# Optimization experiments

Hardware: AMD Instinct MI355X
Metric: run time of the kernel (lower is better)

## Reference

```python
import jax, jax.numpy as jnp
import numpy as np

N = 100000   # nodes
E = 1600000  # edges
EL = 200000  # decode pairs
D_IN, D_HID, D_OUT = 128, 128, 64


def setup_inputs() -> dict:
    key = jax.random.key(0)
    ks = jax.random.split(key, 9)
    x = jax.random.normal(ks[0], (N, D_IN), dtype=jnp.float32)
    edge_index = jax.random.randint(ks[1], (2, E), 0, N, dtype=jnp.int64)
    edge_label_index = jax.random.randint(ks[2], (2, EL), 0, N, dtype=jnp.int64)
    # GCNConv params: weight [in, out] (no bias inside linear), bias added after aggregation
    W1 = jax.random.normal(ks[3], (D_IN, D_HID), dtype=jnp.float32) / np.sqrt(D_IN)
    b1 = jnp.zeros((D_HID,), dtype=jnp.float32)
    W2 = jax.random.normal(ks[4], (D_HID, D_HID), dtype=jnp.float32) / np.sqrt(D_HID)
    b2 = jnp.zeros((D_HID,), dtype=jnp.float32)
    W3 = jax.random.normal(ks[5], (D_HID, D_OUT), dtype=jnp.float32) / np.sqrt(D_HID)
    b3 = jnp.zeros((D_OUT,), dtype=jnp.float32)
    return {"x": x, "edge_index": edge_index, "edge_label_index": edge_label_index,
            "W1": W1, "b1": b1, "W2": W2, "b2": b2, "W3": W3, "b3": b3}


def _gcn_norm(edge_index, num_nodes, dtype):
    # add self-loops, compute symmetric normalization deg^-1/2[src]*deg^-1/2[dst]
    loop = jnp.arange(num_nodes, dtype=edge_index.dtype)
    src = jnp.concatenate([edge_index[0], loop])
    dst = jnp.concatenate([edge_index[1], loop])
    deg = jax.ops.segment_sum(jnp.ones(src.shape, dtype=dtype), dst, num_segments=num_nodes)
    dinv = jax.lax.rsqrt(deg)  # deg >= 1 due to self-loops
    norm = dinv[src] * dinv[dst]
    return src, dst, norm


def _gcn_conv(h, W, b, src, dst, norm, num_nodes):
    h = h @ W                               # [N, out]
    msg = h[src] * norm[:, None]            # gather + scale  [E+N, out]
    out = jax.ops.segment_sum(msg, dst, num_segments=num_nodes)  # scatter-add
    return out + b


def reference(x, edge_index, edge_label_index, W1, b1, W2, b2, W3, b3):
    num_nodes = x.shape[0]
    src, dst, norm = _gcn_norm(edge_index, num_nodes, x.dtype)
    h = jax.nn.relu(_gcn_conv(x, W1, b1, src, dst, norm, num_nodes))
    h = jax.nn.relu(_gcn_conv(h, W2, b2, src, dst, norm, num_nodes))  # dropout is identity in eval
    z = _gcn_conv(h, W3, b3, src, dst, norm, num_nodes)
    # decode: dot product over candidate pairs
    return jnp.sum(z[edge_label_index[0]] * z[edge_label_index[1]], axis=-1)
```

## Files before the change

kernel.cpp:

```cpp
#include <hip/hip_runtime.h>
#include <hip/hip_bf16.h>

#define N_NODES 100000
#define N_EDGES 1600000
#define N_EL    200000

#define CPAD 16
#define GT_GEMM ((N_NODES + 63) / 64)
#define GR_RANK 782
#define GRID_FAT (3 * GR_RANK)
#define NB2 ((N_NODES + 511) / 512)
#define GF_FILL ((N_EDGES + 255) / 256)
#define GF_PRE  ((N_NODES + 1 + 3) / 4)

typedef unsigned int uint32;
typedef unsigned short ushort16;
typedef __attribute__((ext_vector_type(8))) short short8;
typedef __attribute__((ext_vector_type(4))) float f32x4;

static __device__ __forceinline__ ushort16 f2bf(float f) {
    uint32 u = __float_as_uint(f);
    u += 0x7fffu + ((u >> 16) & 1u);
    return (ushort16)(u >> 16);
}
static __device__ __forceinline__ float bf_lo(uint32 p) { return __uint_as_float(p << 16); }
static __device__ __forceinline__ float bf_hi(uint32 p) { return __uint_as_float(p & 0xffff0000u); }
static __device__ __forceinline__ float bf2f(ushort16 h) { return __uint_as_float((uint32)h << 16); }

__global__ void k_scanF(const int* __restrict__ cpad, int* __restrict__ lrp,
                        float* __restrict__ dinv, int* __restrict__ bsum,
                        int* __restrict__ boff, int* __restrict__ cnt) {
    __shared__ int s[512];
    __shared__ int lastflag;
    int t = threadIdx.x;
    int i = blockIdx.x * 512 + t;
    int v = (i < N_NODES) ? cpad[(size_t)i * CPAD] : 0;
    if (i < N_NODES) dinv[i] = 1.0f / sqrtf((float)(v + 1));
    s[t] = v;
    __syncthreads();
    for (int off = 1; off < 512; off <<= 1) {
        int u = (t >= off) ? s[t - off] : 0;
        __syncthreads();
        s[t] += u;
        __syncthreads();
    }
    if (i <= N_NODES) lrp[i] = s[t] - v;
    if (t == 0) {
        __hip_atomic_store(&bsum[blockIdx.x], s[511], __ATOMIC_RELEASE,
                           __HIP_MEMORY_SCOPE_AGENT);
        int c = __hip_atomic_fetch_add(cnt, 1, __ATOMIC_ACQ_REL,
                                       __HIP_MEMORY_SCOPE_AGENT);
        lastflag = (c == NB2 - 1);
    }
    __syncthreads();
    if (!lastflag) return;
    int bv = (t < NB2) ? __hip_atomic_load(&bsum[t], __ATOMIC_ACQUIRE,
                                           __HIP_MEMORY_SCOPE_AGENT) : 0;
    s[t] = bv;
    __syncthreads();
    for (int off = 1; off < 512; off <<= 1) {
        int u = (t >= off) ? s[t - off] : 0;
        __syncthreads();
        s[t] += u;
        __syncthreads();
    }
    if (t < NB2) boff[t] = s[t] - bv;
}

__global__ void k_fill2p(const int* __restrict__ src, const int* __restrict__ dst,
                         const int* __restrict__ lrp, const int* __restrict__ boff,
                         const int* __restrict__ r, int* __restrict__ col,
                         const float* __restrict__ dinv, uint32* __restrict__ t32) {
    unsigned bid = blockIdx.x;
    int tid = threadIdx.x;
    if (bid < GF_FILL) {
        int e = bid * 256 + tid;
        if (e >= N_EDGES) return;
        int dd = dst[e];
        int pos = lrp[dd] + boff[dd >> 9] + r[e];
        __builtin_nontemporal_store(src[e], &col[pos]);
    } else {
        int node = (bid - GF_FILL) * 4 + (tid >> 6);
        int lane = tid & 63;
        if (node > N_NODES) return;
        float di = (node < N_NODES) ? dinv[node] : 0.f;
        size_t idx = (size_t)node * 64 + lane;
        uint32 p = t32[idx];
        float lo = bf_lo(p) * di, hi = bf_hi(p) * di;
        t32[idx] = (uint32)f2bf(lo) | ((uint32)f2bf(hi) << 16);
    }
}

static __device__ __forceinline__ short8 load_afrag(const float* arow, int off) {
    float4 a0 = *(const float4*)(arow + off);
    float4 a1 = *(const float4*)(arow + off + 4);
    short8 af;
    af[0] = (short)f2bf(a0.x); af[1] = (short)f2bf(a0.y);
    af[2] = (short)f2bf(a0.z); af[3] = (short)f2bf(a0.w);
    af[4] = (short)f2bf(a1.x); af[5] = (short)f2bf(a1.y);
    af[6] = (short)f2bf(a1.z); af[7] = (short)f2bf(a1.w);
    return af;
}
static __device__ __forceinline__ short8 load_afrag(const ushort16* arow, int off) {
    return *(const short8*)(arow + off);
}

template <int D, typename AT, bool SCALE, int OS>
static __device__ __forceinline__ void gemm_body(int bid, const AT* __restrict__ A,
        const float* __restrict__ W, const float* __restrict__ dinv,
        ushort16* __restrict__ C) {
    constexpr int NT = D / 16;
    constexpr int LNT = (NT == 8) ? 3 : 2;
    __shared__ short sB[4 * NT * 64 * 8];

    int tid = threadIdx.x;

    constexpr int COMBOS = 4 * 4 * NT * 16;
    for (int cc = tid; cc < COMBOS; cc += 256) {
        int nn = cc & 15;
        int nt = (cc >> 4) & (NT - 1);
        int q  = (cc >> (4 + LNT)) & 3;
        int kt = cc >> (6 + LNT);
        short8 pk;
#pragma unroll
        for (int j = 0; j < 8; ++j)
            pk[j] = (short)f2bf(W[(kt * 32 + q * 8 + j) * D + nt * 16 + nn]);
        *(short8*)&sB[(((kt * NT + nt) * 64) + q * 16 + nn) * 8] = pk;
    }
    __syncthreads();

    int w = tid >> 6;
    int l = tid & 63;
    int q = l >> 4;
    int nn15 = l & 15;
    int m0 = bid * 64 + w * 16;

    f32x4 acc[NT];
#pragma unroll
    for (int i = 0; i < NT; ++i) acc[i] = (f32x4){0.f, 0.f, 0.f, 0.f};

    int m = m0 + nn15;
    m = min(m, N_NODES - 1);
    const AT* arow = A + (size_t)m * 128;

#pragma unroll
    for (int kt = 0; kt < 4; ++kt) {
        short8 af = load_afrag(arow, kt * 32 + q * 8);
#pragma unroll
        for (int nt = 0; nt < NT; ++nt) {
            short8 bf = *(const short8*)&sB[((kt * NT + nt) * 64 + l) * 8];
            acc[nt] = __builtin_amdgcn_mfma_f32_16x16x32_bf16(af, bf, acc[nt], 0, 0, 0);
        }
    }

    float4 dv;
    if constexpr (SCALE) dv = *(const float4*)(dinv + m0 + 4 * q);
    const float* dvp = (const float*)&dv;
#pragma unroll
    for (int nt = 0; nt < NT; ++nt) {
#pragma unroll
        for (int r = 0; r < 4; ++r) {
            int node = m0 + q * 4 + r;
            if (node < N_NODES) {
                float val = acc[nt][r];
                if constexpr (SCALE) val *= dvp[r];
                C[(size_t)node * OS + nt * 16 + nn15] = f2bf(val);
            }
        }
    }
}

template <int D, typename AT, bool SCALE, int OS>
__global__ __launch_bounds__(256, 5) void k_gemm_mfma(const AT* __restrict__ A,
        const float* __restrict__ W, const float* __restrict__ dinv,
        ushort16* __restrict__ C) {
    gemm_body<D, AT, SCALE, OS>(blockIdx.x, A, W, dinv, C);
}

__global__ __launch_bounds__(256, 5) void k_fat1(const float* __restrict__ A,
        const float* __restrict__ W, ushort16* __restrict__ C,
        const int* __restrict__ dst, int* __restrict__ cpad, int* __restrict__ r) {
    unsigned bid = blockIdx.x;
    unsigned g = bid / 3u;
    unsigned rem = bid - g * 3u;
    if (rem < 2u) {
        unsigned gid = g * 2u + rem;
        if (gid < GT_GEMM)
            gemm_body<128, float, false, 128>(gid, A, W, nullptr, C);
    } else {
        unsigned e0 = g * 2048u + threadIdx.x;
        int d[8], rr[8];
#pragma unroll
        for (int k = 0; k < 8; ++k) {
            unsigned e = e0 + k * 256u;
            if (e < N_EDGES) d[k] = dst[e];
        }
#pragma unroll
        for (int k = 0; k < 8; ++k) {
            unsigned e = e0 + k * 256u;
            if (e < N_EDGES) rr[k] = atomicAdd(&cpad[(size_t)d[k] * CPAD], 1);
        }
#pragma unroll
        for (int k = 0; k < 8; ++k) {
            unsigned e = e0 + k * 256u;
            if (e < N_EDGES) __builtin_nontemporal_store(rr[k], &r[e]);
        }
    }
}

template <bool RELU>
__global__ void k_gather128(const int* __restrict__ lrp, const int* __restrict__ boff,
                            const int* __restrict__ col, const float* __restrict__ dinv,
                            const uint32* __restrict__ t, const float* __restrict__ b,
                            uint32* __restrict__ outbuf) {
    __shared__ int sc[4][64];
    int tid = threadIdx.x;
    unsigned wid = (blockIdx.x * 256u + tid) >> 6;
    if (wid >= N_NODES) return;
    int w = tid >> 6;
    int lane = tid & 63;
    int beg = lrp[wid] + boff[wid >> 9];
    int end = lrp[wid + 1] + boff[(wid + 1) >> 9];
    float di = dinv[wid];
    uint32 p = t[(size_t)wid * 64 + lane];
    float ax = bf_lo(p), ay = bf_hi(p);
    for (int base = beg; base < end; base += 64) {
        int cnt = min(end - base, 64);
        int c = N_NODES;
        if (lane < cnt) c = col[base + lane];
        sc[w][lane] = c;
        int nb = (cnt + 7) >> 3;
        for (int j8 = 0; j8 < nb; ++j8) {
            int j = j8 << 3;
            int s0 = sc[w][j+0], s1 = sc[w][j+1], s2 = sc[w][j+2], s3 = sc[w][j+3];
            int s4 = sc[w][j+4], s5 = sc[w][j+5], s6 = sc[w][j+6], s7 = sc[w][j+7];
            uint32 v0 = t[(size_t)s0 * 64 + lane];
            uint32 v1 = t[(size_t)s1 * 64 + lane];
            uint32 v2 = t[(size_t)s2 * 64 + lane];
            uint32 v3 = t[(size_t)s3 * 64 + lane];
            uint32 v4 = t[(size_t)s4 * 64 + lane];
            uint32 v5 = t[(size_t)s5 * 64 + lane];
            uint32 v6 = t[(size_t)s6 * 64 + lane];
            uint32 v7 = t[(size_t)s7 * 64 + lane];
            ax += (bf_lo(v0) + bf_lo(v1)) + (bf_lo(v2) + bf_lo(v3))
                + ((bf_lo(v4) + bf_lo(v5)) + (bf_lo(v6) + bf_lo(v7)));
            ay += (bf_hi(v0) + bf_hi(v1)) + (bf_hi(v2) + bf_hi(v3))
                + ((bf_hi(v4) + bf_hi(v5)) + (bf_hi(v6) + bf_hi(v7)));
        }
    }
    float2 bb = ((const float2*)b)[lane];
    float ox = di * ax + bb.x;
    float oy = di * ay + bb.y;
    if (RELU) { ox = fmaxf(ox, 0.f); oy = fmaxf(oy, 0.f); }
    __builtin_nontemporal_store((uint32)f2bf(ox) | ((uint32)f2bf(oy) << 16),
                                &outbuf[(size_t)wid * 64 + lane]);
}

template <bool RELU>
__global__ void k_gather64(const int* __restrict__ lrp, const int* __restrict__ boff,
                           const int* __restrict__ col, const float* __restrict__ dinv,
                           const ushort16* __restrict__ t, const float* __restrict__ b,
                           ushort16* __restrict__ outbuf) {
    __shared__ int sc[4][64];
    int tid = threadIdx.x;
    unsigned wid = (blockIdx.x * 256u + tid) >> 6;
    if (wid >= N_NODES) return;
    int w = tid >> 6;
    int lane = tid & 63;
    int beg = lrp[wid] + boff[wid >> 9];
    int end = lrp[wid + 1] + boff[(wid + 1) >> 9];
    float di = dinv[wid];
    float acc = bf2f(t[(size_t)wid * 128 + lane]);
    for (int base = beg; base < end; base += 64) {
        int cnt = min(end - base, 64);
        int c = N_NODES;
        if (lane < cnt) c = col[base + lane];
        sc[w][lane] = c;
        int nb = (cnt + 7) >> 3;
        for (int j8 = 0; j8 < nb; ++j8) {
            int j = j8 << 3;
            int s0 = sc[w][j+0], s1 = sc[w][j+1], s2 = sc[w][j+2], s3 = sc[w][j+3];
            int s4 = sc[w][j+4], s5 = sc[w][j+5], s6 = sc[w][j+6], s7 = sc[w][j+7];
            float v0 = bf2f(t[(size_t)s0 * 128 + lane]);
            float v1 = bf2f(t[(size_t)s1 * 128 + lane]);
            float v2 = bf2f(t[(size_t)s2 * 128 + lane]);
            float v3 = bf2f(t[(size_t)s3 * 128 + lane]);
            float v4 = bf2f(t[(size_t)s4 * 128 + lane]);
            float v5 = bf2f(t[(size_t)s5 * 128 + lane]);
            float v6 = bf2f(t[(size_t)s6 * 128 + lane]);
            float v7 = bf2f(t[(size_t)s7 * 128 + lane]);
            acc += (v0 + v1) + (v2 + v3) + ((v4 + v5) + (v6 + v7));
        }
    }
    float o = di * acc + b[lane];
    if (RELU) o = fmaxf(o, 0.f);
    __builtin_nontemporal_store(f2bf(o), &outbuf[(size_t)wid * 64 + lane]);
}

__global__ void k_decode(const int* __restrict__ eli, const ushort16* __restrict__ z,
                         float* __restrict__ out) {
    int e = blockIdx.x * blockDim.x + threadIdx.x;
    if (e >= N_EL) return;
    int a = eli[e];
    int b = eli[N_EL + e];
    const uint4* za = (const uint4*)(z + (size_t)a * 64);
    const uint4* zb = (const uint4*)(z + (size_t)b * 64);
    float acc = 0.0f;
#pragma unroll
    for (int i = 0; i < 8; ++i) {
        uint4 va = za[i], vb = zb[i];
        acc += bf_lo(va.x) * bf_lo(vb.x) + bf_hi(va.x) * bf_hi(vb.x);
        acc += bf_lo(va.y) * bf_lo(vb.y) + bf_hi(va.y) * bf_hi(vb.y);
        acc += bf_lo(va.z) * bf_lo(vb.z) + bf_hi(va.z) * bf_hi(vb.z);
        acc += bf_lo(va.w) * bf_lo(vb.w) + bf_hi(va.w) * bf_hi(vb.w);
    }
    out[e] = acc;
}

extern "C" void kernel_launch(void* const* d_in, const int* in_sizes, int n_in,
                              void* d_out, int out_size, void* d_ws, size_t ws_size,
                              hipStream_t stream) {
    const float* x   = (const float*)d_in[0];
    const int*   ei  = (const int*)d_in[1];
    const int*   eli = (const int*)d_in[2];
    const float* W1  = (const float*)d_in[3];
    const float* b1  = (const float*)d_in[4];
    const float* W2  = (const float*)d_in[5];
    const float* b2  = (const float*)d_in[6];
    const float* W3  = (const float*)d_in[7];
    const float* b3  = (const float*)d_in[8];
    float* out = (float*)d_out;

    const int* srcA = ei;
    const int* dstA = ei + N_EDGES;

    char* ws = (char*)d_ws;
    float*    dinv   = (float*)   (ws + 0);
    int*      lrp    = (int*)     (ws + (1024u << 10));
    int*      bsum   = (int*)     (ws + (1888u << 10));
    int*      boff   = (int*)     (ws + (1896u << 10));
    int*      col    = (int*)     (ws + (2048u << 10));
    int*      r      = (int*)     (ws + (9u << 20));
    ushort16* t      = (ushort16*)(ws + (16u << 20));
    ushort16* aggb   = (ushort16*)(ws + (48u << 20));
    int*      cpad   = (int*)     (ws + (80u << 20));
    int*      cnt    = cpad + (size_t)N_NODES * CPAD;

    const int B = 256;
    const int gG  = (N_NODES * 64 + B - 1) / B;
    const int gEL = (N_EL + B - 1) / B;

    hipMemsetAsync(cpad, 0, ((size_t)N_NODES * CPAD + 16) * sizeof(int), stream);
    k_fat1<<<GRID_FAT, B, 0, stream>>>(x, W1, t, dstA, cpad, r);
    k_scanF<<<NB2, 512, 0, stream>>>(cpad, lrp, dinv, bsum, boff, cnt);
    k_fill2p<<<GF_FILL + GF_PRE, B, 0, stream>>>(srcA, dstA, lrp, boff, r, col,
                                                 dinv, (uint32*)t);

    k_gather128<true><<<gG, B, 0, stream>>>(lrp, boff, col, dinv, (const uint32*)t,
                                            b1, (uint32*)aggb);
    k_gemm_mfma<128, ushort16, true, 128><<<GT_GEMM, B, 0, stream>>>(aggb, W2, dinv, t);
    k_gather128<true><<<gG, B, 0, stream>>>(lrp, boff, col, dinv, (const uint32*)t,
                                            b2, (uint32*)aggb);
    k_gemm_mfma<64, ushort16, true, 128><<<GT_GEMM, B, 0, stream>>>(aggb, W3, dinv, t);
    k_gather64<false><<<gG, B, 0, stream>>>(lrp, boff, col, dinv, t, b3, aggb);

    k_decode<<<gEL, B, 0, stream>>>(eli, aggb, out);
}
```

Baseline: 437.2 us.

## Build CSR via two-level bucket sort and widen gather loads

```diff
diff --git a/kernel.cpp b/kernel.cpp
--- a/kernel.cpp
+++ b/kernel.cpp
@@ -5,13 +5,12 @@
 #define N_EDGES 1600000
 #define N_EL    200000
 
-#define CPAD 16
+#define NBKT 782
+#define NCHK 782
+#define CHKE 2048
+#define DCAP 2688
 #define GT_GEMM ((N_NODES + 63) / 64)
-#define GR_RANK 782
-#define GRID_FAT (3 * GR_RANK)
-#define NB2 ((N_NODES + 511) / 512)
-#define GF_FILL ((N_EDGES + 255) / 256)
-#define GF_PRE  ((N_NODES + 1 + 3) / 4)
+#define GRID_FAT (3 * NCHK)
 
 typedef unsigned int uint32;
 typedef unsigned short ushort16;
@@ -25,69 +24,147 @@
 }
 static __device__ __forceinline__ float bf_lo(uint32 p) { return __uint_as_float(p << 16); }
 static __device__ __forceinline__ float bf_hi(uint32 p) { return __uint_as_float(p & 0xffff0000u); }
-static __device__ __forceinline__ float bf2f(ushort16 h) { return __uint_as_float((uint32)h << 16); }
-
-__global__ void k_scanF(const int* __restrict__ cpad, int* __restrict__ lrp,
-                        float* __restrict__ dinv, int* __restrict__ bsum,
-                        int* __restrict__ boff, int* __restrict__ cnt) {
-    __shared__ int s[512];
+static __device__ __forceinline__ uint32 pack2(float lo, float hi) {
+    return (uint32)f2bf(lo) | ((uint32)f2bf(hi) << 16);
+}
+
+template <bool AT>
+static __device__ __forceinline__ int scan782(const int* __restrict__ in,
+                                              int* __restrict__ outv,
+                                              int* s, int tid) {
+    __syncthreads();
+    int v[4]; int sum = 0;
+    int i0 = tid * 4;
+#pragma unroll
+    for (int i = 0; i < 4; ++i) {
+        int idx = i0 + i;
+        int x = 0;
+        if (idx < NBKT)
+            x = AT ? __hip_atomic_load(&in[idx], __ATOMIC_ACQUIRE,
+                                       __HIP_MEMORY_SCOPE_AGENT)
+                   : in[idx];
+        v[i] = x; sum += x;
+    }
+    s[tid] = sum;
+    __syncthreads();
+    for (int off = 1; off < 256; off <<= 1) {
+        int u = (tid >= off) ? s[tid - off] : 0;
+        __syncthreads();
+        s[tid] += u;
+        __syncthreads();
+    }
+    int excl = s[tid] - sum;
+    int total = s[255];
+    int run = excl;
+#pragma unroll
+    for (int i = 0; i < 4; ++i) {
+        int idx = i0 + i;
+        if (idx < NBKT) outv[idx] = run;
+        run += v[i];
+    }
+    return total;
+}
+
+__global__ __launch_bounds__(256) void k_scanB(const int* __restrict__ H,
+        int* __restrict__ CO, int* __restrict__ TT, int* __restrict__ BB,
+        int* __restrict__ cnt) {
+    __shared__ int s[256];
     __shared__ int lastflag;
-    int t = threadIdx.x;
-    int i = blockIdx.x * 512 + t;
-    int v = (i < N_NODES) ? cpad[(size_t)i * CPAD] : 0;
-    if (i < N_NODES) dinv[i] = 1.0f / sqrtf((float)(v + 1));
-    s[t] = v;
-    __syncthreads();
-    for (int off = 1; off < 512; off <<= 1) {
-        int u = (t >= off) ? s[t - off] : 0;
-        __syncthreads();
-        s[t] += u;
-        __syncthreads();
-    }
-    if (i <= N_NODES) lrp[i] = s[t] - v;
-    if (t == 0) {
-        __hip_atomic_store(&bsum[blockIdx.x], s[511], __ATOMIC_RELEASE,
-                           __HIP_MEMORY_SCOPE_AGENT);
+    int b = blockIdx.x, tid = threadIdx.x;
+    int total = scan782<false>(H + (size_t)b * NBKT, CO + (size_t)b * NBKT, s, tid);
+    if (tid == 0) {
+        __hip_atomic_store(&TT[b], total, __ATOMIC_RELEASE, __HIP_MEMORY_SCOPE_AGENT);
         int c = __hip_atomic_fetch_add(cnt, 1, __ATOMIC_ACQ_REL,
                                        __HIP_MEMORY_SCOPE_AGENT);
-        lastflag = (c == NB2 - 1);
+        lastflag = (c == NBKT - 1);
     }
     __syncthreads();
     if (!lastflag) return;
-    int bv = (t < NB2) ? __hip_atomic_load(&bsum[t], __ATOMIC_ACQUIRE,
-                                           __HIP_MEMORY_SCOPE_AGENT) : 0;
-    s[t] = bv;
-    __syncthreads();
-    for (int off = 1; off < 512; off <<= 1) {
-        int u = (t >= off) ? s[t - off] : 0;
-        __syncthreads();
-        s[t] += u;
-        __syncthreads();
-    }
-    if (t < NB2) boff[t] = s[t] - bv;
-}
-
-__global__ void k_fill2p(const int* __restrict__ src, const int* __restrict__ dst,
-                         const int* __restrict__ lrp, const int* __restrict__ boff,
-                         const int* __restrict__ r, int* __restrict__ col,
-                         const float* __restrict__ dinv, uint32* __restrict__ t32) {
-    unsigned bid = blockIdx.x;
-    int tid = threadIdx.x;
-    if (bid < GF_FILL) {
-        int e = bid * 256 + tid;
-        if (e >= N_EDGES) return;
-        int dd = dst[e];
-        int pos = lrp[dd] + boff[dd >> 9] + r[e];
-        __builtin_nontemporal_store(src[e], &col[pos]);
-    } else {
-        int node = (bid - GF_FILL) * 4 + (tid >> 6);
-        int lane = tid & 63;
-        if (node > N_NODES) return;
-        float di = (node < N_NODES) ? dinv[node] : 0.f;
-        size_t idx = (size_t)node * 64 + lane;
-        uint32 p = t32[idx];
-        float lo = bf_lo(p) * di, hi = bf_hi(p) * di;
-        t32[idx] = (uint32)f2bf(lo) | ((uint32)f2bf(hi) << 16);
+    int gt = scan782<true>(TT, BB, s, tid);
+    __syncthreads();
+    if (tid == 0) BB[NBKT] = gt;
+}
+
+__global__ __launch_bounds__(256) void k_csrC(const int* __restrict__ src,
+        const int* __restrict__ dst, const int* __restrict__ CO,
+        const int* __restrict__ BB, long long* __restrict__ ed) {
+    __shared__ int cur[NBKT];
+    int c = blockIdx.x, tid = threadIdx.x;
+    for (int i = tid; i < NBKT; i += 256)
+        cur[i] = BB[i] + CO[(size_t)i * NBKT + c];
+    __syncthreads();
+    int e0 = c * CHKE;
+#pragma unroll
+    for (int kk = 0; kk < 8; ++kk) {
+        int e = e0 + kk * 256 + tid;
+        if (e < N_EDGES) {
+            int sE = src[e], dE = dst[e];
+            int pos = atomicAdd(&cur[dE >> 7], 1);
+            long long pv = (unsigned int)sE | ((long long)(unsigned int)dE << 32);
+            __builtin_nontemporal_store(pv, &ed[pos]);
+        }
+    }
+}
+
+__global__ __launch_bounds__(256) void k_csrD(const long long* __restrict__ ed,
+        const int* __restrict__ BB, int* __restrict__ rowptr,
+        float* __restrict__ dinv, int* __restrict__ col, uint32* __restrict__ t32) {
+    __shared__ long long eds[DCAP];
+    __shared__ int deg[128], scn[128], cur[128];
+    __shared__ float dv[128];
+    int b = blockIdx.x, tid = threadIdx.x;
+    int base = BB[b], lim = BB[b + 1];
+    int n = lim - base;
+    bool cached = (n <= DCAP);
+    if (tid < 128) deg[tid] = 0;
+    __syncthreads();
+    for (int i = tid; i < n; i += 256) {
+        long long e = ed[base + i];
+        if (cached) eds[i] = e;
+        int d = (int)(e >> 32);
+        atomicAdd(&deg[d & 127], 1);
+    }
+    __syncthreads();
+    if (tid < 128) scn[tid] = deg[tid];
+    __syncthreads();
+    for (int off = 1; off < 128; off <<= 1) {
+        int u = 0;
+        if (tid < 128 && tid >= off) u = scn[tid - off];
+        __syncthreads();
+        if (tid < 128) scn[tid] += u;
+        __syncthreads();
+    }
+    if (tid < 128) {
+        int excl = scn[tid] - deg[tid];
+        cur[tid] = excl;
+        int node = b * 128 + tid;
+        if (node < N_NODES) {
+            rowptr[node] = base + excl;
+            float di = rsqrtf((float)(deg[tid] + 1));
+            dinv[node] = di;
+            dv[tid] = di;
+        }
+    }
+    if (b == NBKT - 1 && tid == 0) rowptr[N_NODES] = BB[NBKT];
+    __syncthreads();
+    for (int i = tid; i < n; i += 256) {
+        long long e = cached ? eds[i] : ed[base + i];
+        int sE = (int)(e & 0xffffffff);
+        int d = (int)(e >> 32);
+        int p = atomicAdd(&cur[d & 127], 1);
+        col[base + p] = sE;
+    }
+    __syncthreads();
+    for (int idx = tid; idx < 128 * 64; idx += 256) {
+        int ni = idx >> 6;
+        int node = b * 128 + ni;
+        if (node < N_NODES) {
+            int k = idx & 63;
+            size_t a = (size_t)node * 64 + k;
+            uint32 p = t32[a];
+            float di = dv[ni];
+            t32[a] = pack2(bf_lo(p) * di, bf_hi(p) * di);
+        }
     }
 }
 
@@ -108,11 +185,9 @@
 template <int D, typename AT, bool SCALE, int OS>
 static __device__ __forceinline__ void gemm_body(int bid, const AT* __restrict__ A,
         const float* __restrict__ W, const float* __restrict__ dinv,
-        ushort16* __restrict__ C) {
+        ushort16* __restrict__ C, short* sB) {
     constexpr int NT = D / 16;
     constexpr int LNT = (NT == 8) ? 3 : 2;
-    __shared__ short sB[4 * NT * 64 * 8];
-
     int tid = threadIdx.x;
 
     constexpr int COMBOS = 4 * 4 * NT * 16;
@@ -153,9 +228,9 @@
         }
     }
 
-    float4 dv;
-    if constexpr (SCALE) dv = *(const float4*)(dinv + m0 + 4 * q);
-    const float* dvp = (const float*)&dv;
+    float4 dvv;
+    if constexpr (SCALE) dvv = *(const float4*)(dinv + m0 + 4 * q);
+    const float* dvp = (const float*)&dvv;
 #pragma unroll
     for (int nt = 0; nt < NT; ++nt) {
 #pragma unroll
@@ -174,56 +249,56 @@
 __global__ __launch_bounds__(256, 5) void k_gemm_mfma(const AT* __restrict__ A,
         const float* __restrict__ W, const float* __restrict__ dinv,
         ushort16* __restrict__ C) {
-    gemm_body<D, AT, SCALE, OS>(blockIdx.x, A, W, dinv, C);
+    __shared__ short sB[4 * (D / 16) * 64 * 8];
+    gemm_body<D, AT, SCALE, OS>(blockIdx.x, A, W, dinv, C, sB);
 }
 
 __global__ __launch_bounds__(256, 5) void k_fat1(const float* __restrict__ A,
         const float* __restrict__ W, ushort16* __restrict__ C,
-        const int* __restrict__ dst, int* __restrict__ cpad, int* __restrict__ r) {
+        const int* __restrict__ dst, int* __restrict__ H) {
+    __shared__ __align__(16) char smem[32768];
     unsigned bid = blockIdx.x;
     unsigned g = bid / 3u;
     unsigned rem = bid - g * 3u;
+    int tid = threadIdx.x;
     if (rem < 2u) {
         unsigned gid = g * 2u + rem;
         if (gid < GT_GEMM)
-            gemm_body<128, float, false, 128>(gid, A, W, nullptr, C);
+            gemm_body<128, float, false, 128>(gid, A, W, nullptr, C, (short*)smem);
     } else {
-        unsigned e0 = g * 2048u + threadIdx.x;
-        int d[8], rr[8];
-#pragma unroll
-        for (int k = 0; k < 8; ++k) {
-            unsigned e = e0 + k * 256u;
-            if (e < N_EDGES) d[k] = dst[e];
-        }
-#pragma unroll
-        for (int k = 0; k < 8; ++k) {
-            unsigned e = e0 + k * 256u;
-            if (e < N_EDGES) rr[k] = atomicAdd(&cpad[(size_t)d[k] * CPAD], 1);
-        }
-#pragma unroll
-        for (int k = 0; k < 8; ++k) {
-            unsigned e = e0 + k * 256u;
-            if (e < N_EDGES) __builtin_nontemporal_store(rr[k], &r[e]);
-        }
+        int* hist = (int*)smem;
+        for (int i = tid; i < NBKT; i += 256) hist[i] = 0;
+        __syncthreads();
+        int e0 = (int)g * CHKE;
+#pragma unroll
+        for (int kk = 0; kk < 8; ++kk) {
+            int e = e0 + kk * 256 + tid;
+            if (e < N_EDGES) atomicAdd(&hist[dst[e] >> 7], 1);
+        }
+        __syncthreads();
+        for (int i = tid; i < NBKT; i += 256)
+            H[(size_t)i * NBKT + g] = hist[i];
     }
 }
 
 template <bool RELU>
-__global__ void k_gather128(const int* __restrict__ lrp, const int* __restrict__ boff,
-                            const int* __restrict__ col, const float* __restrict__ dinv,
-                            const uint32* __restrict__ t, const float* __restrict__ b,
-                            uint32* __restrict__ outbuf) {
+__global__ void k_gather128(const int* __restrict__ rowptr, const int* __restrict__ col,
+                            const float* __restrict__ dinv, const uint32* __restrict__ t,
+                            const float* __restrict__ b, uint32* __restrict__ outbuf) {
     __shared__ int sc[4][64];
     int tid = threadIdx.x;
     unsigned wid = (blockIdx.x * 256u + tid) >> 6;
     if (wid >= N_NODES) return;
     int w = tid >> 6;
     int lane = tid & 63;
-    int beg = lrp[wid] + boff[wid >> 9];
-    int end = lrp[wid + 1] + boff[(wid + 1) >> 9];
-    float di = dinv[wid];
-    uint32 p = t[(size_t)wid * 64 + lane];
-    float ax = bf_lo(p), ay = bf_hi(p);
+    int h = lane >> 5;
+    int k = lane & 31;
+    int beg = rowptr[wid], end = rowptr[wid + 1];
+    float a0 = 0.f, a1 = 0.f, a2 = 0.f, a3 = 0.f;
+    if (h == 0) {
+        uint2 p = ((const uint2*)(t + (size_t)wid * 64))[k];
+        a0 = bf_lo(p.x); a1 = bf_hi(p.x); a2 = bf_lo(p.y); a3 = bf_hi(p.y);
+    }
     for (int base = beg; base < end; base += 64) {
         int cnt = min(end - base, 64);
         int c = N_NODES;
@@ -232,45 +307,59 @@
         int nb = (cnt + 7) >> 3;
         for (int j8 = 0; j8 < nb; ++j8) {
             int j = j8 << 3;
-            int s0 = sc[w][j+0], s1 = sc[w][j+1], s2 = sc[w][j+2], s3 = sc[w][j+3];
-            int s4 = sc[w][j+4], s5 = sc[w][j+5], s6 = sc[w][j+6], s7 = sc[w][j+7];
-            uint32 v0 = t[(size_t)s0 * 64 + lane];
-            uint32 v1 = t[(size_t)s1 * 64 + lane];
-            uint32 v2 = t[(size_t)s2 * 64 + lane];
-            uint32 v3 = t[(size_t)s3 * 64 + lane];
-            uint32 v4 = t[(size_t)s4 * 64 + lane];
-            uint32 v5 = t[(size_t)s5 * 64 + lane];
-            uint32 v6 = t[(size_t)s6 * 64 + lane];
-            uint32 v7 = t[(size_t)s7 * 64 + lane];
-            ax += (bf_lo(v0) + bf_lo(v1)) + (bf_lo(v2) + bf_lo(v3))
-                + ((bf_lo(v4) + bf_lo(v5)) + (bf_lo(v6) + bf_lo(v7)));
-            ay += (bf_hi(v0) + bf_hi(v1)) + (bf_hi(v2) + bf_hi(v3))
-                + ((bf_hi(v4) + bf_hi(v5)) + (bf_hi(v6) + bf_hi(v7)));
-        }
-    }
-    float2 bb = ((const float2*)b)[lane];
-    float ox = di * ax + bb.x;
-    float oy = di * ay + bb.y;
-    if (RELU) { ox = fmaxf(ox, 0.f); oy = fmaxf(oy, 0.f); }
-    __builtin_nontemporal_store((uint32)f2bf(ox) | ((uint32)f2bf(oy) << 16),
-                                &outbuf[(size_t)wid * 64 + lane]);
-}
-
-template <bool RELU>
-__global__ void k_gather64(const int* __restrict__ lrp, const int* __restrict__ boff,
-                           const int* __restrict__ col, const float* __restrict__ dinv,
-                           const ushort16* __restrict__ t, const float* __restrict__ b,
-                           ushort16* __restrict__ outbuf) {
+            int r0 = sc[w][j + 0 + h];
+            int r1 = sc[w][j + 2 + h];
+            int r2 = sc[w][j + 4 + h];
+            int r3 = sc[w][j + 6 + h];
+            uint2 v0 = ((const uint2*)(t + (size_t)r0 * 64))[k];
+            uint2 v1 = ((const uint2*)(t + (size_t)r1 * 64))[k];
+            uint2 v2 = ((const uint2*)(t + (size_t)r2 * 64))[k];
+            uint2 v3 = ((const uint2*)(t + (size_t)r3 * 64))[k];
+            a0 += (bf_lo(v0.x) + bf_lo(v1.x)) + (bf_lo(v2.x) + bf_lo(v3.x));
+            a1 += (bf_hi(v0.x) + bf_hi(v1.x)) + (bf_hi(v2.x) + bf_hi(v3.x));
+            a2 += (bf_lo(v0.y) + bf_lo(v1.y)) + (bf_lo(v2.y) + bf_lo(v3.y));
+            a3 += (bf_hi(v0.y) + bf_hi(v1.y)) + (bf_hi(v2.y) + bf_hi(v3.y));
+        }
+    }
+    a0 += __shfl_xor(a0, 32);
+    a1 += __shfl_xor(a1, 32);
+    a2 += __shfl_xor(a2, 32);
+    a3 += __shfl_xor(a3, 32);
+    if (h == 0) {
+        float di = dinv[wid];
+        float4 bb = ((const float4*)b)[k];
+        float o0 = fmaf(di, a0, bb.x);
+        float o1 = fmaf(di, a1, bb.y);
+        float o2 = fmaf(di, a2, bb.z);
+        float o3 = fmaf(di, a3, bb.w);
+        if (RELU) {
+            o0 = fmaxf(o0, 0.f); o1 = fmaxf(o1, 0.f);
+            o2 = fmaxf(o2, 0.f); o3 = fmaxf(o3, 0.f);
+        }
+        unsigned long long pv = (unsigned long long)pack2(o0, o1)
+                              | ((unsigned long long)pack2(o2, o3) << 32);
+        __builtin_nontemporal_store(pv,
+            (unsigned long long*)(outbuf + (size_t)wid * 64) + k);
+    }
+}
+
+__global__ void k_gather64(const int* __restrict__ rowptr, const int* __restrict__ col,
+                           const float* __restrict__ dinv, const uint32* __restrict__ t,
+                           const float* __restrict__ b, uint32* __restrict__ outbuf) {
     __shared__ int sc[4][64];
     int tid = threadIdx.x;
     unsigned wid = (blockIdx.x * 256u + tid) >> 6;
     if (wid >= N_NODES) return;
     int w = tid >> 6;
     int lane = tid & 63;
-    int beg = lrp[wid] + boff[wid >> 9];
-    int end = lrp[wid + 1] + boff[(wid + 1) >> 9];
-    float di = dinv[wid];
-    float acc = bf2f(t[(size_t)wid * 128 + lane]);
+    int h = lane >> 4;
+    int k = lane & 15;
+    int beg = rowptr[wid], end = rowptr[wid + 1];
+    float a0 = 0.f, a1 = 0.f, a2 = 0.f, a3 = 0.f;
+    if (h == 0) {
+        uint2 p = ((const uint2*)(t + (size_t)wid * 64))[k];
+        a0 = bf_lo(p.x); a1 = bf_hi(p.x); a2 = bf_lo(p.y); a3 = bf_hi(p.y);
+    }
     for (int base = beg; base < end; base += 64) {
         int cnt = min(end - base, 64);
         int c = N_NODES;
@@ -279,22 +368,32 @@
         int nb = (cnt + 7) >> 3;
         for (int j8 = 0; j8 < nb; ++j8) {
             int j = j8 << 3;
-            int s0 = sc[w][j+0], s1 = sc[w][j+1], s2 = sc[w][j+2], s3 = sc[w][j+3];
-            int s4 = sc[w][j+4], s5 = sc[w][j+5], s6 = sc[w][j+6], s7 = sc[w][j+7];
-            float v0 = bf2f(t[(size_t)s0 * 128 + lane]);
-            float v1 = bf2f(t[(size_t)s1 * 128 + lane]);
-            float v2 = bf2f(t[(size_t)s2 * 128 + lane]);
-            float v3 = bf2f(t[(size_t)s3 * 128 + lane]);
-            float v4 = bf2f(t[(size_t)s4 * 128 + lane]);
-            float v5 = bf2f(t[(size_t)s5 * 128 + lane]);
-            float v6 = bf2f(t[(size_t)s6 * 128 + lane]);
-            float v7 = bf2f(t[(size_t)s7 * 128 + lane]);
-            acc += (v0 + v1) + (v2 + v3) + ((v4 + v5) + (v6 + v7));
-        }
-    }
-    float o = di * acc + b[lane];
-    if (RELU) o = fmaxf(o, 0.f);
-    __builtin_nontemporal_store(f2bf(o), &outbuf[(size_t)wid * 64 + lane]);
+            int r0 = sc[w][j + h];
+            int r1 = sc[w][j + 4 + h];
+            uint2 v0 = ((const uint2*)(t + (size_t)r0 * 64))[k];
+            uint2 v1 = ((const uint2*)(t + (size_t)r1 * 64))[k];
+            a0 += bf_lo(v0.x) + bf_lo(v1.x);
+            a1 += bf_hi(v0.x) + bf_hi(v1.x);
+            a2 += bf_lo(v0.y) + bf_lo(v1.y);
+            a3 += bf_hi(v0.y) + bf_hi(v1.y);
+        }
+    }
+    a0 += __shfl_xor(a0, 16); a0 += __shfl_xor(a0, 32);
+    a1 += __shfl_xor(a1, 16); a1 += __shfl_xor(a1, 32);
+    a2 += __shfl_xor(a2, 16); a2 += __shfl_xor(a2, 32);
+    a3 += __shfl_xor(a3, 16); a3 += __shfl_xor(a3, 32);
+    if (h == 0) {
+        float di = dinv[wid];
+        float4 bb = ((const float4*)b)[k];
+        float o0 = fmaf(di, a0, bb.x);
+        float o1 = fmaf(di, a1, bb.y);
+        float o2 = fmaf(di, a2, bb.z);
+        float o3 = fmaf(di, a3, bb.w);
+        unsigned long long pv = (unsigned long long)pack2(o0, o1)
+                              | ((unsigned long long)pack2(o2, o3) << 32);
+        __builtin_nontemporal_store(pv,
+            (unsigned long long*)(outbuf + (size_t)wid * 32) + k);
+    }
 }
 
 __global__ void k_decode(const int* __restrict__ eli, const ushort16* __restrict__ z,
@@ -335,34 +434,38 @@
     const int* dstA = ei + N_EDGES;
 
     char* ws = (char*)d_ws;
-    float*    dinv   = (float*)   (ws + 0);
-    int*      lrp    = (int*)     (ws + (1024u << 10));
-    int*      bsum   = (int*)     (ws + (1888u << 10));
-    int*      boff   = (int*)     (ws + (1896u << 10));
-    int*      col    = (int*)     (ws + (2048u << 10));
-    int*      r      = (int*)     (ws + (9u << 20));
-    ushort16* t      = (ushort16*)(ws + (16u << 20));
-    ushort16* aggb   = (ushort16*)(ws + (48u << 20));
-    int*      cpad   = (int*)     (ws + (80u << 20));
-    int*      cnt    = cpad + (size_t)N_NODES * CPAD;
+    float*      dinv   = (float*)    (ws + 0);
+    int*        rowptr = (int*)      (ws + (1024u << 10));
+    int*        TT     = (int*)      (ws + (1536u << 10));
+    int*        BB     = (int*)      (ws + (1638u << 10));
+    int*        cnt    = (int*)      (ws + (1792u << 10));
+    int*        col    = (int*)      (ws + (2048u << 10));
+    int*        H      = (int*)      (ws + (9u << 20));
+    int*        CO     = (int*)      (ws + (12u << 20));
+    long long*  ed     = (long long*)(ws + (16u << 20));
+    ushort16*   t      = (ushort16*) (ws + (32u << 20));
+    ushort16*   aggb   = (ushort16*) (ws + (60u << 20));
 
     const int B = 256;
     const int gG  = (N_NODES * 64 + B - 1) / B;
     const int gEL = (N_EL + B - 1) / B;
 
-    hipMemsetAsync(cpad, 0, ((size_t)N_NODES * CPAD + 16) * sizeof(int), stream);
-    k_fat1<<<GRID_FAT, B, 0, stream>>>(x, W1, t, dstA, cpad, r);
-    k_scanF<<<NB2, 512, 0, stream>>>(cpad, lrp, dinv, bsum, boff, cnt);
-    k_fill2p<<<GF_FILL + GF_PRE, B, 0, stream>>>(srcA, dstA, lrp, boff, r, col,
-                                                 dinv, (uint32*)t);
-
-    k_gather128<true><<<gG, B, 0, stream>>>(lrp, boff, col, dinv, (const uint32*)t,
+    hipMemsetAsync(cnt, 0, 4, stream);
+    hipMemsetAsync((char*)t + (size_t)N_NODES * 256, 0, 256, stream);
+
+    k_fat1<<<GRID_FAT, B, 0, stream>>>(x, W1, t, dstA, H);
+    k_scanB<<<NBKT, B, 0, stream>>>(H, CO, TT, BB, cnt);
+    k_csrC<<<NCHK, B, 0, stream>>>(srcA, dstA, CO, BB, ed);
+    k_csrD<<<NBKT, B, 0, stream>>>(ed, BB, rowptr, dinv, col, (uint32*)t);
+
+    k_gather128<true><<<gG, B, 0, stream>>>(rowptr, col, dinv, (const uint32*)t,
                                             b1, (uint32*)aggb);
     k_gemm_mfma<128, ushort16, true, 128><<<GT_GEMM, B, 0, stream>>>(aggb, W2, dinv, t);
-    k_gather128<true><<<gG, B, 0, stream>>>(lrp, boff, col, dinv, (const uint32*)t,
+    k_gather128<true><<<gG, B, 0, stream>>>(rowptr, col, dinv, (const uint32*)t,
                                             b2, (uint32*)aggb);
     k_gemm_mfma<64, ushort16, true, 128><<<GT_GEMM, B, 0, stream>>>(aggb, W3, dinv, t);
-    k_gather64<false><<<gG, B, 0, stream>>>(lrp, boff, col, dinv, t, b3, aggb);
+    k_gather64<<<gG, B, 0, stream>>>(rowptr, col, dinv, (const uint32*)t, b3,
+                                     (uint32*)aggb);
 
     k_decode<<<gEL, B, 0, stream>>>(eli, aggb, out);
 }
```

Measured after the change: 461.7 us. +5.6%, slower.

## Split gather rows across half-waves, fold dinv scaling into first gather, compact layer-3 output

Applied to the files above, without the earlier changes.

```diff
diff --git a/kernel.cpp b/kernel.cpp
--- a/kernel.cpp
+++ b/kernel.cpp
@@ -7,11 +7,8 @@
 
 #define CPAD 16
 #define GT_GEMM ((N_NODES + 63) / 64)
-#define GR_RANK 782
-#define GRID_FAT (3 * GR_RANK)
+#define GE_RANK ((N_EDGES + 255) / 256)
 #define NB2 ((N_NODES + 511) / 512)
-#define GF_FILL ((N_EDGES + 255) / 256)
-#define GF_PRE  ((N_NODES + 1 + 3) / 4)
 
 typedef unsigned int uint32;
 typedef unsigned short ushort16;
@@ -25,7 +22,9 @@
 }
 static __device__ __forceinline__ float bf_lo(uint32 p) { return __uint_as_float(p << 16); }
 static __device__ __forceinline__ float bf_hi(uint32 p) { return __uint_as_float(p & 0xffff0000u); }
-static __device__ __forceinline__ float bf2f(ushort16 h) { return __uint_as_float((uint32)h << 16); }
+static __device__ __forceinline__ uint32 pack2(float lo, float hi) {
+    return (uint32)f2bf(lo) | ((uint32)f2bf(hi) << 16);
+}
 
 __global__ void k_scanF(const int* __restrict__ cpad, int* __restrict__ lrp,
                         float* __restrict__ dinv, int* __restrict__ bsum,
@@ -35,7 +34,7 @@
     int t = threadIdx.x;
     int i = blockIdx.x * 512 + t;
     int v = (i < N_NODES) ? cpad[(size_t)i * CPAD] : 0;
-    if (i < N_NODES) dinv[i] = 1.0f / sqrtf((float)(v + 1));
+    if (i < N_NODES) dinv[i] = rsqrtf((float)(v + 1));
     s[t] = v;
     __syncthreads();
     for (int off = 1; off < 512; off <<= 1) {
@@ -67,28 +66,14 @@
     if (t < NB2) boff[t] = s[t] - bv;
 }
 
-__global__ void k_fill2p(const int* __restrict__ src, const int* __restrict__ dst,
-                         const int* __restrict__ lrp, const int* __restrict__ boff,
-                         const int* __restrict__ r, int* __restrict__ col,
-                         const float* __restrict__ dinv, uint32* __restrict__ t32) {
-    unsigned bid = blockIdx.x;
-    int tid = threadIdx.x;
-    if (bid < GF_FILL) {
-        int e = bid * 256 + tid;
-        if (e >= N_EDGES) return;
-        int dd = dst[e];
-        int pos = lrp[dd] + boff[dd >> 9] + r[e];
-        __builtin_nontemporal_store(src[e], &col[pos]);
-    } else {
-        int node = (bid - GF_FILL) * 4 + (tid >> 6);
-        int lane = tid & 63;
-        if (node > N_NODES) return;
-        float di = (node < N_NODES) ? dinv[node] : 0.f;
-        size_t idx = (size_t)node * 64 + lane;
-        uint32 p = t32[idx];
-        float lo = bf_lo(p) * di, hi = bf_hi(p) * di;
-        t32[idx] = (uint32)f2bf(lo) | ((uint32)f2bf(hi) << 16);
-    }
+__global__ void k_fill2(const int* __restrict__ src, const int* __restrict__ dst,
+                        const int* __restrict__ lrp, const int* __restrict__ boff,
+                        const int* __restrict__ r, int* __restrict__ col) {
+    int e = blockIdx.x * blockDim.x + threadIdx.x;
+    if (e >= N_EDGES) return;
+    int dd = dst[e];
+    int pos = lrp[dd] + boff[dd >> 9] + r[e];
+    __builtin_nontemporal_store(src[e], &col[pos]);
 }
 
 static __device__ __forceinline__ short8 load_afrag(const float* arow, int off) {
@@ -108,11 +93,9 @@
 template <int D, typename AT, bool SCALE, int OS>
 static __device__ __forceinline__ void gemm_body(int bid, const AT* __restrict__ A,
         const float* __restrict__ W, const float* __restrict__ dinv,
-        ushort16* __restrict__ C) {
+        ushort16* __restrict__ C, short* sB) {
     constexpr int NT = D / 16;
     constexpr int LNT = (NT == 8) ? 3 : 2;
-    __shared__ short sB[4 * NT * 64 * 8];
-
     int tid = threadIdx.x;
 
     constexpr int COMBOS = 4 * 4 * NT * 16;
@@ -153,148 +136,185 @@
         }
     }
 
-    float4 dv;
-    if constexpr (SCALE) dv = *(const float4*)(dinv + m0 + 4 * q);
-    const float* dvp = (const float*)&dv;
+    float4 dvv;
+    if constexpr (SCALE) dvv = *(const float4*)(dinv + m0 + 4 * q);
+    const float* dvp = (const float*)&dvv;
 #pragma unroll
     for (int nt = 0; nt < NT; ++nt) {
 #pragma unroll
-        for (int r = 0; r < 4; ++r) {
-            int node = m0 + q * 4 + r;
+        for (int rr = 0; rr < 4; ++rr) {
+            int node = m0 + q * 4 + rr;
             if (node < N_NODES) {
-                float val = acc[nt][r];
-                if constexpr (SCALE) val *= dvp[r];
+                float val = acc[nt][rr];
+                if constexpr (SCALE) val *= dvp[rr];
                 C[(size_t)node * OS + nt * 16 + nn15] = f2bf(val);
             }
         }
     }
 }
 
-template <int D, typename AT, bool SCALE, int OS>
+template <int D, typename AT, bool SCALE, int OS, bool PADZ>
 __global__ __launch_bounds__(256, 5) void k_gemm_mfma(const AT* __restrict__ A,
         const float* __restrict__ W, const float* __restrict__ dinv,
         ushort16* __restrict__ C) {
-    gemm_body<D, AT, SCALE, OS>(blockIdx.x, A, W, dinv, C);
+    __shared__ short sB[4 * (D / 16) * 64 * 8];
+    if (PADZ && blockIdx.x == 0 && threadIdx.x < OS / 2)
+        ((uint32*)C)[(size_t)N_NODES * (OS / 2) + threadIdx.x] = 0;
+    gemm_body<D, AT, SCALE, OS>(blockIdx.x, A, W, dinv, C, sB);
 }
 
 __global__ __launch_bounds__(256, 5) void k_fat1(const float* __restrict__ A,
         const float* __restrict__ W, ushort16* __restrict__ C,
         const int* __restrict__ dst, int* __restrict__ cpad, int* __restrict__ r) {
+    __shared__ short sB[4 * 8 * 64 * 8];
     unsigned bid = blockIdx.x;
-    unsigned g = bid / 3u;
-    unsigned rem = bid - g * 3u;
-    if (rem < 2u) {
-        unsigned gid = g * 2u + rem;
-        if (gid < GT_GEMM)
-            gemm_body<128, float, false, 128>(gid, A, W, nullptr, C);
+    unsigned g = bid / 5u;
+    unsigned rem = bid - g * 5u;
+    if (rem == 0u) {
+        gemm_body<128, float, false, 128>(g, A, W, nullptr, C, sB);
     } else {
-        unsigned e0 = g * 2048u + threadIdx.x;
-        int d[8], rr[8];
-#pragma unroll
-        for (int k = 0; k < 8; ++k) {
-            unsigned e = e0 + k * 256u;
-            if (e < N_EDGES) d[k] = dst[e];
-        }
-#pragma unroll
-        for (int k = 0; k < 8; ++k) {
-            unsigned e = e0 + k * 256u;
-            if (e < N_EDGES) rr[k] = atomicAdd(&cpad[(size_t)d[k] * CPAD], 1);
-        }
-#pragma unroll
-        for (int k = 0; k < 8; ++k) {
-            unsigned e = e0 + k * 256u;
-            if (e < N_EDGES) __builtin_nontemporal_store(rr[k], &r[e]);
-        }
-    }
-}
-
-template <bool RELU>
+        unsigned rid = g * 4u + rem - 1u;
+        unsigned e = rid * 256u + threadIdx.x;
+        if (e < N_EDGES) r[e] = atomicAdd(&cpad[(size_t)dst[e] * CPAD], 1);
+    }
+}
+
+template <bool RELU, bool WEIGHTED>
 __global__ void k_gather128(const int* __restrict__ lrp, const int* __restrict__ boff,
                             const int* __restrict__ col, const float* __restrict__ dinv,
                             const uint32* __restrict__ t, const float* __restrict__ b,
                             uint32* __restrict__ outbuf) {
+    __shared__ int   sc[4][64];
+    __shared__ float sd[4][64];
+    int tid = threadIdx.x;
+    unsigned wid = (blockIdx.x * 256u + tid) >> 6;
+    if (wid >= N_NODES) return;
+    int w = tid >> 6;
+    int lane = tid & 63;
+    int h = lane >> 5;
+    int k = lane & 31;
+    int beg = lrp[wid] + boff[wid >> 9];
+    int end = lrp[wid + 1] + boff[(wid + 1) >> 9];
+    float di = dinv[wid];
+    float a0 = 0.f, a1 = 0.f, a2 = 0.f, a3 = 0.f;
+    if (h == 0) {
+        uint2 p = ((const uint2*)(t + (size_t)wid * 64))[k];
+        float sw = WEIGHTED ? di : 1.0f;
+        a0 = sw * bf_lo(p.x); a1 = sw * bf_hi(p.x);
+        a2 = sw * bf_lo(p.y); a3 = sw * bf_hi(p.y);
+    }
+    for (int base = beg; base < end; base += 64) {
+        int cnt = min(end - base, 64);
+        int c = WEIGHTED ? 0 : N_NODES;
+        if (lane < cnt) c = col[base + lane];
+        sc[w][lane] = c;
+        if (WEIGHTED) sd[w][lane] = (lane < cnt) ? dinv[c] : 0.f;
+        int nb8 = (cnt + 7) >> 3;
+        for (int j8 = 0; j8 < nb8; ++j8) {
+            int j = j8 << 3;
+            int r0 = sc[w][j + 0 + h];
+            int r1 = sc[w][j + 2 + h];
+            int r2 = sc[w][j + 4 + h];
+            int r3 = sc[w][j + 6 + h];
+            uint2 v0 = ((const uint2*)(t + (size_t)r0 * 64))[k];
+            uint2 v1 = ((const uint2*)(t + (size_t)r1 * 64))[k];
+            uint2 v2 = ((const uint2*)(t + (size_t)r2 * 64))[k];
+            uint2 v3 = ((const uint2*)(t + (size_t)r3 * 64))[k];
+            if (WEIGHTED) {
+                float d0 = sd[w][j + 0 + h];
+                float d1 = sd[w][j + 2 + h];
+                float d2 = sd[w][j + 4 + h];
+                float d3 = sd[w][j + 6 + h];
+                a0 = fmaf(d0, bf_lo(v0.x), a0); a1 = fmaf(d0, bf_hi(v0.x), a1);
+                a2 = fmaf(d0, bf_lo(v0.y), a2); a3 = fmaf(d0, bf_hi(v0.y), a3);
+                a0 = fmaf(d1, bf_lo(v1.x), a0); a1 = fmaf(d1, bf_hi(v1.x), a1);
+                a2 = fmaf(d1, bf_lo(v1.y), a2); a3 = fmaf(d1, bf_hi(v1.y), a3);
+                a0 = fmaf(d2, bf_lo(v2.x), a0); a1 = fmaf(d2, bf_hi(v2.x), a1);
+                a2 = fmaf(d2, bf_lo(v2.y), a2); a3 = fmaf(d2, bf_hi(v2.y), a3);
+                a0 = fmaf(d3, bf_lo(v3.x), a0); a1 = fmaf(d3, bf_hi(v3.x), a1);
+                a2 = fmaf(d3, bf_lo(v3.y), a2); a3 = fmaf(d3, bf_hi(v3.y), a3);
+            } else {
+                a0 += (bf_lo(v0.x) + bf_lo(v1.x)) + (bf_lo(v2.x) + bf_lo(v3.x));
+                a1 += (bf_hi(v0.x) + bf_hi(v1.x)) + (bf_hi(v2.x) + bf_hi(v3.x));
+                a2 += (bf_lo(v0.y) + bf_lo(v1.y)) + (bf_lo(v2.y) + bf_lo(v3.y));
+                a3 += (bf_hi(v0.y) + bf_hi(v1.y)) + (bf_hi(v2.y) + bf_hi(v3.y));
+            }
+        }
+    }
+    a0 += __shfl_xor(a0, 32);
+    a1 += __shfl_xor(a1, 32);
+    a2 += __shfl_xor(a2, 32);
+    a3 += __shfl_xor(a3, 32);
+    if (h == 0) {
+        float4 bb = ((const float4*)b)[k];
+        float o0 = fmaf(di, a0, bb.x);
+        float o1 = fmaf(di, a1, bb.y);
+        float o2 = fmaf(di, a2, bb.z);
+        float o3 = fmaf(di, a3, bb.w);
+        if (RELU) {
+            o0 = fmaxf(o0, 0.f); o1 = fmaxf(o1, 0.f);
+            o2 = fmaxf(o2, 0.f); o3 = fmaxf(o3, 0.f);
+        }
+        unsigned long long pv = (unsigned long long)pack2(o0, o1)
+                              | ((unsigned long long)pack2(o2, o3) << 32);
+        __builtin_nontemporal_store(pv,
+            (unsigned long long*)(outbuf + (size_t)wid * 64) + k);
+    }
+}
+
+__global__ void k_gather64(const int* __restrict__ lrp, const int* __restrict__ boff,
+                           const int* __restrict__ col, const float* __restrict__ dinv,
+                           const uint32* __restrict__ z, const float* __restrict__ b,
+                           uint32* __restrict__ outbuf) {
     __shared__ int sc[4][64];
     int tid = threadIdx.x;
     unsigned wid = (blockIdx.x * 256u + tid) >> 6;
     if (wid >= N_NODES) return;
     int w = tid >> 6;
     int lane = tid & 63;
+    int h = lane >> 4;
+    int k = lane & 15;
     int beg = lrp[wid] + boff[wid >> 9];
     int end = lrp[wid + 1] + boff[(wid + 1) >> 9];
-    float di = dinv[wid];
-    uint32 p = t[(size_t)wid * 64 + lane];
-    float ax = bf_lo(p), ay = bf_hi(p);
+    float a0 = 0.f, a1 = 0.f, a2 = 0.f, a3 = 0.f;
+    if (h == 0) {
+        uint2 p = ((const uint2*)(z + (size_t)wid * 32))[k];
+        a0 = bf_lo(p.x); a1 = bf_hi(p.x); a2 = bf_lo(p.y); a3 = bf_hi(p.y);
+    }
     for (int base = beg; base < end; base += 64) {
         int cnt = min(end - base, 64);
         int c = N_NODES;
         if (lane < cnt) c = col[base + lane];
         sc[w][lane] = c;
-        int nb = (cnt + 7) >> 3;
-        for (int j8 = 0; j8 < nb; ++j8) {
+        int nb8 = (cnt + 7) >> 3;
+        for (int j8 = 0; j8 < nb8; ++j8) {
             int j = j8 << 3;
-            int s0 = sc[w][j+0], s1 = sc[w][j+1], s2 = sc[w][j+2], s3 = sc[w][j+3];
-            int s4 = sc[w][j+4], s5 = sc[w][j+5], s6 = sc[w][j+6], s7 = sc[w][j+7];
-            uint32 v0 = t[(size_t)s0 * 64 + lane];
-            uint32 v1 = t[(size_t)s1 * 64 + lane];
-            uint32 v2 = t[(size_t)s2 * 64 + lane];
-            uint32 v3 = t[(size_t)s3 * 64 + lane];
-            uint32 v4 = t[(size_t)s4 * 64 + lane];
-            uint32 v5 = t[(size_t)s5 * 64 + lane];
-            uint32 v6 = t[(size_t)s6 * 64 + lane];
-            uint32 v7 = t[(size_t)s7 * 64 + lane];
-            ax += (bf_lo(v0) + bf_lo(v1)) + (bf_lo(v2) + bf_lo(v3))
-                + ((bf_lo(v4) + bf_lo(v5)) + (bf_lo(v6) + bf_lo(v7)));
-            ay += (bf_hi(v0) + bf_hi(v1)) + (bf_hi(v2) + bf_hi(v3))
-                + ((bf_hi(v4) + bf_hi(v5)) + (bf_hi(v6) + bf_hi(v7)));
-        }
-    }
-    float2 bb = ((const float2*)b)[lane];
-    float ox = di * ax + bb.x;
-    float oy = di * ay + bb.y;
-    if (RELU) { ox = fmaxf(ox, 0.f); oy = fmaxf(oy, 0.f); }
-    __builtin_nontemporal_store((uint32)f2bf(ox) | ((uint32)f2bf(oy) << 16),
-                                &outbuf[(size_t)wid * 64 + lane]);
-}
-
-template <bool RELU>
-__global__ void k_gather64(const int* __restrict__ lrp, const int* __restrict__ boff,
-                           const int* __restrict__ col, const float* __restrict__ dinv,
-                           const ushort16* __restrict__ t, const float* __restrict__ b,
-                           ushort16* __restrict__ outbuf) {
-    __shared__ int sc[4][64];
-    int tid = threadIdx.x;
-    unsigned wid = (blockIdx.x * 256u + tid) >> 6;
-    if (wid >= N_NODES) return;
-    int w = tid >> 6;
-    int lane = tid & 63;
-    int beg = lrp[wid] + boff[wid >> 9];
-    int end = lrp[wid + 1] + boff[(wid + 1) >> 9];
-    float di = dinv[wid];
-    float acc = bf2f(t[(size_t)wid * 128 + lane]);
-    for (int base = beg; base < end; base += 64) {
-        int cnt = min(end - base, 64);
-        int c = N_NODES;
-        if (lane < cnt) c = col[base + lane];
-        sc[w][lane] = c;
-        int nb = (cnt + 7) >> 3;
-        for (int j8 = 0; j8 < nb; ++j8) {
-            int j = j8 << 3;
-            int s0 = sc[w][j+0], s1 = sc[w][j+1], s2 = sc[w][j+2], s3 = sc[w][j+3];
-            int s4 = sc[w][j+4], s5 = sc[w][j+5], s6 = sc[w][j+6], s7 = sc[w][j+7];
-            float v0 = bf2f(t[(size_t)s0 * 128 + lane]);
-            float v1 = bf2f(t[(size_t)s1 * 128 + lane]);
-            float v2 = bf2f(t[(size_t)s2 * 128 + lane]);
-            float v3 = bf2f(t[(size_t)s3 * 128 + lane]);
-            float v4 = bf2f(t[(size_t)s4 * 128 + lane]);
-            float v5 = bf2f(t[(size_t)s5 * 128 + lane]);
-            float v6 = bf2f(t[(size_t)s6 * 128 + lane]);
-            float v7 = bf2f(t[(size_t)s7 * 128 + lane]);
-            acc += (v0 + v1) + (v2 + v3) + ((v4 + v5) + (v6 + v7));
-        }
-    }
-    float o = di * acc + b[lane];
-    if (RELU) o = fmaxf(o, 0.f);
-    __builtin_nontemporal_store(f2bf(o), &outbuf[(size_t)wid * 64 + lane]);
+            int r0 = sc[w][j + h];
+            int r1 = sc[w][j + 4 + h];
+            uint2 v0 = ((const uint2*)(z + (size_t)r0 * 32))[k];
+            uint2 v1 = ((const uint2*)(z + (size_t)r1 * 32))[k];
+            a0 += bf_lo(v0.x) + bf_lo(v1.x);
+            a1 += bf_hi(v0.x) + bf_hi(v1.x);
+            a2 += bf_lo(v0.y) + bf_lo(v1.y);
+            a3 += bf_hi(v0.y) + bf_hi(v1.y);
+        }
+    }
+    a0 += __shfl_xor(a0, 16); a0 += __shfl_xor(a0, 32);
+    a1 += __shfl_xor(a1, 16); a1 += __shfl_xor(a1, 32);
+    a2 += __shfl_xor(a2, 16); a2 += __shfl_xor(a2, 32);
+    a3 += __shfl_xor(a3, 16); a3 += __shfl_xor(a3, 32);
+    if (h == 0) {
+        float di = dinv[wid];
+        float4 bb = ((const float4*)b)[k];
+        float o0 = fmaf(di, a0, bb.x);
+        float o1 = fmaf(di, a1, bb.y);
+        float o2 = fmaf(di, a2, bb.z);
+        float o3 = fmaf(di, a3, bb.w);
+        unsigned long long pv = (unsigned long long)pack2(o0, o1)
+                              | ((unsigned long long)pack2(o2, o3) << 32);
+        __builtin_nontemporal_store(pv,
+            (unsigned long long*)(outbuf + (size_t)wid * 32) + k);
+    }
 }
 
 __global__ void k_decode(const int* __restrict__ eli, const ushort16* __restrict__ z,
@@ -351,18 +371,21 @@
     const int gEL = (N_EL + B - 1) / B;
 
     hipMemsetAsync(cpad, 0, ((size_t)N_NODES * CPAD + 16) * sizeof(int), stream);
-    k_fat1<<<GRID_FAT, B, 0, stream>>>(x, W1, t, dstA, cpad, r);
+    hipMemsetAsync((char*)t + (size_t)N_NODES * 256, 0, 256, stream);
+    k_fat1<<<GT_GEMM + GE_RANK, B, 0, stream>>>(x, W1, t, dstA, cpad, r);
     k_scanF<<<NB2, 512, 0, stream>>>(cpad, lrp, dinv, bsum, boff, cnt);
-    k_fill2p<<<GF_FILL + GF_PRE, B, 0, stream>>>(srcA, dstA, lrp, boff, r, col,
-                                                 dinv, (uint32*)t);
-
-    k_gather128<true><<<gG, B, 0, stream>>>(lrp, boff, col, dinv, (const uint32*)t,
-                                            b1, (uint32*)aggb);
-    k_gemm_mfma<128, ushort16, true, 128><<<GT_GEMM, B, 0, stream>>>(aggb, W2, dinv, t);
-    k_gather128<true><<<gG, B, 0, stream>>>(lrp, boff, col, dinv, (const uint32*)t,
-                                            b2, (uint32*)aggb);
-    k_gemm_mfma<64, ushort16, true, 128><<<GT_GEMM, B, 0, stream>>>(aggb, W3, dinv, t);
-    k_gather64<false><<<gG, B, 0, stream>>>(lrp, boff, col, dinv, t, b3, aggb);
+    k_fill2<<<GE_RANK, B, 0, stream>>>(srcA, dstA, lrp, boff, r, col);
+
+    k_gather128<true, true><<<gG, B, 0, stream>>>(lrp, boff, col, dinv,
+                                                  (const uint32*)t, b1, (uint32*)aggb);
+    k_gemm_mfma<128, ushort16, true, 128, false><<<GT_GEMM, B, 0, stream>>>(
+        aggb, W2, dinv, t);
+    k_gather128<true, false><<<gG, B, 0, stream>>>(lrp, boff, col, dinv,
+                                                   (const uint32*)t, b2, (uint32*)aggb);
+    k_gemm_mfma<64, ushort16, true, 64, true><<<GT_GEMM, B, 0, stream>>>(
+        aggb, W3, dinv, t);
+    k_gather64<<<gG, B, 0, stream>>>(lrp, boff, col, dinv, (const uint32*)t, b3,
+                                     (uint32*)aggb);
 
     k_decode<<<gEL, B, 0, stream>>>(eli, aggb, out);
 }
```

Result: no change. 444.0 us (+1.6%).
